# Performance work log

Hardware: AMD Instinct MI355X
Metric: run time of the kernel (lower is better)

## Reference

```python
import jax, jax.numpy as jnp
import numpy as np

B, N, M = 4, 16384, 4096
C1, C2 = 256, 512
C_IN = C1 + C2  # 768
C_H, C_OUT = 256, 256
EPS_BN = 1e-5
EPS_DIST = 1e-8


def _bn(x, gamma, beta):
    # x: [B, C, n]; training-mode batchnorm (batch statistics over B and n)
    mean = x.mean(axis=(0, 2), keepdims=True)
    var = x.var(axis=(0, 2), keepdims=True)
    return (x - mean) * jax.lax.rsqrt(var + EPS_BN) * gamma[None, :, None] + beta[None, :, None]


def setup_inputs() -> dict:
    key = jax.random.key(0)
    ks = jax.random.split(key, 8)
    inp = {
        "unknown": jax.random.normal(ks[0], (B, N, 3), dtype=jnp.float32),
        "known": jax.random.normal(ks[1], (B, M, 3), dtype=jnp.float32),
        "unknow_feats": jax.random.normal(ks[2], (B, C1, N), dtype=jnp.float32),
        "known_feats": jax.random.normal(ks[3], (B, C2, M), dtype=jnp.float32),
        "W1": jax.random.normal(ks[4], (C_H, C_IN), dtype=jnp.float32) * 0.02,
        "b1": jnp.zeros((C_H,), dtype=jnp.float32),
        "g1": jnp.ones((C_H,), dtype=jnp.float32),
        "bt1": jnp.zeros((C_H,), dtype=jnp.float32),
        "W2": jax.random.normal(ks[5], (C_OUT, C_H), dtype=jnp.float32) * 0.02,
        "b2": jnp.zeros((C_OUT,), dtype=jnp.float32),
        "g2": jnp.ones((C_OUT,), dtype=jnp.float32),
        "bt2": jnp.zeros((C_OUT,), dtype=jnp.float32),
    }
    return inp


def reference(unknown, known, unknow_feats, known_feats,
              W1, b1, g1, bt1, W2, b2, g2, bt2):
    # --- three_nn: brute-force squared distances [B, n, m], take 3 smallest ---
    d2 = jnp.sum((unknown[:, :, None, :] - known[:, None, :, :]) ** 2, axis=-1)
    neg_d, idx = jax.lax.top_k(-d2, 3)          # idx: [B, n, 3]
    dist = -neg_d                                # squared dists (as in CUDA three_nn)
    recip = 1.0 / (dist + EPS_DIST)
    weight = recip / recip.sum(axis=-1, keepdims=True)  # [B, n, 3]
    # --- three_interpolate: weighted gather from known_feats [B, C2, m] ---
    gathered = jax.vmap(lambda f, i: f[:, i])(known_feats, idx)  # [B, C2, n, 3]
    interp = jnp.einsum('bcnk,bnk->bcn', gathered, weight)       # [B, C2, n]
    # --- concat + SharedMLP (1x1 conv -> BN -> ReLU, twice) ---
    x = jnp.concatenate([interp, unknow_feats], axis=1)          # [B, C1+C2, n]
    x = jax.nn.relu(_bn(jnp.einsum('bcn,oc->bon', x, W1) + b1[None, :, None], g1, bt1))
    x = jax.nn.relu(_bn(jnp.einsum('bcn,oc->bon', x, W2) + b2[None, :, None], g2, bt2))
    return x  # [B, mlp[-1], n]
```

## Files before the change

kernel.cpp:

```cpp
#include <hip/hip_runtime.h>
#include <hip/hip_bf16.h>
#include <stdint.h>
#include <stddef.h>

#define B_   4
#define N_   16384
#define M_   4096
#define C1_  256
#define C2_  512
#define CIN_ 768
#define CH_  256
#define NG_  (B_*N_)
#define NSLOT 64

typedef __attribute__((ext_vector_type(8))) short short8;
typedef __attribute__((ext_vector_type(4))) float f32x4;

__device__ __forceinline__ float bf2f(unsigned short u){
  union { unsigned int i; float f; } v; v.i = ((unsigned int)u)<<16; return v.f;
}
__device__ __forceinline__ unsigned short f2bf(float f){
  union { float f; unsigned int i; } v; v.f = f;
  unsigned int r = v.i + 0x7fffu + ((v.i>>16)&1u);
  return (unsigned short)(r>>16);
}

__global__ __launch_bounds__(256) void prep_k(const float* __restrict__ W1,
                                              const float* __restrict__ W2,
                                              const float* __restrict__ kn,
                                              unsigned short* __restrict__ W1b,
                                              unsigned short* __restrict__ W2b,
                                              float4* __restrict__ k4){
  int i = blockIdx.x*256 + threadIdx.x;
  if (i < CIN_*CH_) W1b[i] = f2bf(W1[i]);
  if (i < CH_*CH_)  W2b[i] = f2bf(W2[i]);
  if (i < B_*M_){
    float x = kn[3*i], y = kn[3*i+1], z = kn[3*i+2];
    float4 v; v.x = -2.f*x; v.y = -2.f*y; v.z = -2.f*z; v.w = x*x+y*y+z*z;
    k4[i] = v;
  }
}

__global__ __launch_bounds__(256) void kft_k(const float* __restrict__ kf,
                                             unsigned short* __restrict__ kftb){
  int m0 = blockIdx.x*64, c0 = blockIdx.y*64, b = blockIdx.z;
  __shared__ float tile[64][65];
  int t = threadIdx.x;
  #pragma unroll
  for (int p=0;p<16;p++){
    int row = p*4 + (t>>6), col = t&63;
    tile[row][col] = kf[((size_t)b*C2_ + c0+row)*M_ + m0+col];
  }
  __syncthreads();
  #pragma unroll
  for (int q=0;q<2;q++){
    int id = q*256 + t;
    int ml = id >> 3, c8 = (id & 7)*8;
    short8 o;
    #pragma unroll
    for (int e=0;e<8;++e) o[e] = (short)f2bf(tile[c8+e][ml]);
    *(short8*)(kftb + ((size_t)b*M_ + m0+ml)*C2_ + c0 + c8) = o;
  }
}

__global__ __launch_bounds__(512) void three_nn_k(const float* __restrict__ unk,
                                                  const float4* __restrict__ k4,
                                                  int* __restrict__ idx,
                                                  float* __restrict__ wgt){
  __shared__ __align__(16) char smem[65536];
  float4* kl = (float4*)smem;
  float*  sd = (float*)smem;
  int*    si = (int*)(smem + 24*128*4);
  int b  = blockIdx.x >> 7;
  int n0 = (blockIdx.x & 127) * 128;
  int t = threadIdx.x;
  int w = t >> 6, l = t & 63;
  const float4* src = k4 + (size_t)b*M_;
  #pragma unroll
  for (int i=0;i<8;++i) kl[i*512 + t] = src[i*512 + t];
  const float* upA = unk + ((size_t)b*N_ + n0 + l)*3;
  const float* upB = unk + ((size_t)b*N_ + n0 + 64 + l)*3;
  float ax=upA[0], ay=upA[1], az=upA[2];
  float bx=upB[0], by=upB[1], bz=upB[2];
  __syncthreads();
  float a0=1e30f,a1=1e30f,a2=1e30f; int ia0=0,ia1=0,ia2=0;
  float b0=1e30f,b1=1e30f,b2=1e30f; int ib0=0,ib1=0,ib2=0;
  const float4* kp = kl + w*512;
  const int mbase = w*512;
  #pragma unroll 8
  for (int m=0;m<512;++m){
    float4 kq = kp[m];
    int mi = mbase + m;
    float da = __builtin_fmaf(ax,kq.x, __builtin_fmaf(ay,kq.y, __builtin_fmaf(az,kq.z, kq.w)));
    float db = __builtin_fmaf(bx,kq.x, __builtin_fmaf(by,kq.y, __builtin_fmaf(bz,kq.z, kq.w)));
    {
      bool c0 = da < a0, c1 = da < a1, c2 = da < a2;
      int tA = c1 ? ia1 : mi;  ia2 = c2 ? tA : ia2;
      int tB = c0 ? ia0 : mi;  ia1 = c1 ? tB : ia1;
      ia0 = c0 ? mi : ia0;
      float n1 = __builtin_amdgcn_fmed3f(da, a0, a1);
      float n2 = __builtin_amdgcn_fmed3f(da, a1, a2);
      a0 = fminf(da, a0); a1 = n1; a2 = n2;
    }
    {
      bool c0 = db < b0, c1 = db < b1, c2 = db < b2;
      int tA = c1 ? ib1 : mi;  ib2 = c2 ? tA : ib2;
      int tB = c0 ? ib0 : mi;  ib1 = c1 ? tB : ib1;
      ib0 = c0 ? mi : ib0;
      float n1 = __builtin_amdgcn_fmed3f(db, b0, b1);
      float n2 = __builtin_amdgcn_fmed3f(db, b1, b2);
      b0 = fminf(db, b0); b1 = n1; b2 = n2;
    }
  }
  __syncthreads();
  sd[(w*3+0)*128 + l] = a0;  sd[(w*3+0)*128 + 64 + l] = b0;
  sd[(w*3+1)*128 + l] = a1;  sd[(w*3+1)*128 + 64 + l] = b1;
  sd[(w*3+2)*128 + l] = a2;  sd[(w*3+2)*128 + 64 + l] = b2;
  si[(w*3+0)*128 + l] = ia0; si[(w*3+0)*128 + 64 + l] = ib0;
  si[(w*3+1)*128 + l] = ia1; si[(w*3+1)*128 + 64 + l] = ib1;
  si[(w*3+2)*128 + l] = ia2; si[(w*3+2)*128 + 64 + l] = ib2;
  __syncthreads();
  if (t < 128) {
    float bd0=1e30f,bd1=1e30f,bd2=1e30f; int bi0=0,bi1=0,bi2=0;
    #pragma unroll
    for (int q=0;q<24;++q){
      float d = sd[q*128 + t]; int ii = si[q*128 + t];
      bool c0 = d < bd0, c1 = d < bd1, c2 = d < bd2;
      int tA = c1 ? bi1 : ii;  bi2 = c2 ? tA : bi2;
      int tB = c0 ? bi0 : ii;  bi1 = c1 ? tB : bi1;
      bi0 = c0 ? ii : bi0;
      float nd1 = __builtin_amdgcn_fmed3f(d, bd0, bd1);
      float nd2 = __builtin_amdgcn_fmed3f(d, bd1, bd2);
      bd0 = fminf(d, bd0); bd1 = nd1; bd2 = nd2;
    }
    int np = n0 + t;
    const float* upt = unk + ((size_t)b*N_ + np)*3;
    float x = upt[0], y = upt[1], z = upt[2];
    float uu0 = x*x + y*y + z*z;
    float t0 = fmaxf(bd0 + uu0, 0.f) + 1e-8f;
    float t1 = fmaxf(bd1 + uu0, 0.f) + 1e-8f;
    float t2 = fmaxf(bd2 + uu0, 0.f) + 1e-8f;
    float r0 = 1.f/t0, r1 = 1.f/t1, r2 = 1.f/t2;
    float s = r0+r1+r2;
    size_t gp = ((size_t)b*N_ + np)*3;
    idx[gp]=bi0; idx[gp+1]=bi1; idx[gp+2]=bi2;
    wgt[gp]=r0/s; wgt[gp+1]=r1/s; wgt[gp+2]=r2/s;
  }
}

__global__ __launch_bounds__(256) void build_xt_k(const float* __restrict__ uf,
                                                  const unsigned short* __restrict__ kftb,
                                                  const int* __restrict__ idx,
                                                  const float* __restrict__ wgt,
                                                  unsigned short* __restrict__ Xt){
  int b  = blockIdx.x >> 8;
  int n0 = (blockIdx.x & 255) * 64;
  int t = threadIdx.x;
  __shared__ float tile[64][65];
  for (int cc=0; cc<4; ++cc){
    int c0 = cc*64;
    __syncthreads();
    #pragma unroll
    for (int p=0;p<16;p++){
      int row = p*4 + (t>>6), col = t&63;
      tile[row][col] = uf[((size_t)b*C1_ + c0+row)*N_ + n0+col];
    }
    __syncthreads();
    #pragma unroll
    for (int q=0;q<2;q++){
      int id = q*256 + t;
      int nl = id >> 3, c8 = (id & 7)*8;
      short8 o;
      #pragma unroll
      for (int e=0;e<8;++e) o[e] = (short)f2bf(tile[c8+e][nl]);
      *(short8*)(Xt + ((size_t)b*N_ + n0+nl)*CIN_ + C2_ + c0 + c8) = o;
    }
  }
  int w = t>>6, l = t&63;
  for (int i=0;i<16;++i){
    int n = n0 + w*16 + i;
    size_t gp = ((size_t)b*N_ + n)*3;
    int   j0 = idx[gp],   j1 = idx[gp+1],   j2 = idx[gp+2];
    float w0 = wgt[gp],   w1 = wgt[gp+1],   w2 = wgt[gp+2];
    const short8 a0 = *(const short8*)(kftb + ((size_t)b*M_ + j0)*C2_ + l*8);
    const short8 a1 = *(const short8*)(kftb + ((size_t)b*M_ + j1)*C2_ + l*8);
    const short8 a2 = *(const short8*)(kftb + ((size_t)b*M_ + j2)*C2_ + l*8);
    short8 o;
    #pragma unroll
    for (int e=0;e<8;++e){
      float f = w0*bf2f((unsigned short)a0[e])
              + w1*bf2f((unsigned short)a1[e])
              + w2*bf2f((unsigned short)a2[e]);
      o[e] = (short)f2bf(f);
    }
    *(short8*)(Xt + ((size_t)b*N_ + n)*CIN_ + l*8) = o;
  }
}

template<int KTOT, bool AFF>
__global__ __launch_bounds__(256) void gemm_bt_k(const unsigned short* __restrict__ Wb,
                                                 const unsigned short* __restrict__ Bt,
                                                 unsigned short* __restrict__ Yt,
                                                 float* __restrict__ sump,
                                                 float* __restrict__ sqp,
                                                 const float* __restrict__ scalep,
                                                 const float* __restrict__ shiftp){
  __shared__ short lsA[128*64];
  __shared__ short lsB[128*64];
  const int t = threadIdx.x, w = t>>6, l = t&63;
  const int nBase = blockIdx.x*128, oBase = blockIdx.y*128;
  const int wm = w>>1, wn = w&1, rl = l&15, hi = l>>4;
  f32x4 acc[4][4];
  #pragma unroll
  for (int i=0;i<4;i++)
    #pragma unroll
    for (int j=0;j<4;j++) acc[i][j] = (f32x4){0.f,0.f,0.f,0.f};
  const int srow8 = l>>3, sch = l&7;
  for (int ks=0; ks<KTOT/64; ++ks){
    const int k0 = ks*64;
    __syncthreads();
    #pragma unroll
    for (int j=0;j<4;++j){
      int row = w*8 + j*32 + srow8;
      const unsigned short* gA = Wb + (size_t)(oBase+row)*KTOT + k0 + ((sch ^ (row&7))<<3);
      __builtin_amdgcn_global_load_lds((const __attribute__((address_space(1))) unsigned int*)gA,
          (__attribute__((address_space(3))) unsigned int*)(lsA + w*512 + j*2048), 16, 0, 0);
      if constexpr (!AFF){
        const unsigned short* gB = Bt + (size_t)(nBase+row)*KTOT + k0 + ((sch ^ (row&7))<<3);
        __builtin_amdgcn_global_load_lds((const __attribute__((address_space(1))) unsigned int*)gB,
            (__attribute__((address_space(3))) unsigned int*)(lsB + w*512 + j*2048), 16, 0, 0);
      }
    }
    if constexpr (AFF){
      #pragma unroll
      for (int j=0;j<4;++j){
        int row = w*8 + j*32 + srow8;
        int chb = k0 + ((sch ^ (row&7))<<3);
        const short8 v = *(const short8*)(Bt + (size_t)(nBase+row)*KTOT + chb);
        float4 sc0 = *(const float4*)(scalep + chb);
        float4 sc1 = *(const float4*)(scalep + chb + 4);
        float4 sh0 = *(const float4*)(shiftp + chb);
        float4 sh1 = *(const float4*)(shiftp + chb + 4);
        short8 o;
        float f0 = bf2f((unsigned short)v[0])*sc0.x + sh0.x; o[0] = (short)f2bf(f0 > 0.f ? f0 : 0.f);
        float f1 = bf2f((unsigned short)v[1])*sc0.y + sh0.y; o[1] = (short)f2bf(f1 > 0.f ? f1 : 0.f);
        float f2 = bf2f((unsigned short)v[2])*sc0.z + sh0.z; o[2] = (short)f2bf(f2 > 0.f ? f2 : 0.f);
        float f3 = bf2f((unsigned short)v[3])*sc0.w + sh0.w; o[3] = (short)f2bf(f3 > 0.f ? f3 : 0.f);
        float f4 = bf2f((unsigned short)v[4])*sc1.x + sh1.x; o[4] = (short)f2bf(f4 > 0.f ? f4 : 0.f);
        float f5 = bf2f((unsigned short)v[5])*sc1.y + sh1.y; o[5] = (short)f2bf(f5 > 0.f ? f5 : 0.f);
        float f6 = bf2f((unsigned short)v[6])*sc1.z + sh1.z; o[6] = (short)f2bf(f6 > 0.f ? f6 : 0.f);
        float f7 = bf2f((unsigned short)v[7])*sc1.w + sh1.w; o[7] = (short)f2bf(f7 > 0.f ? f7 : 0.f);
        *(short8*)(lsB + w*512 + j*2048 + l*8) = o;
      }
    }
    __syncthreads();
    #pragma unroll
    for (int kk=0;kk<2;++kk){
      short8 af[4], bfr[4];
      const int pc = ((kk*4 + hi) ^ (rl&7)) << 3;
      #pragma unroll
      for (int mi=0;mi<4;++mi) af[mi]  = *(const short8*)(lsA + (wm*64 + mi*16 + rl)*64 + pc);
      #pragma unroll
      for (int ni=0;ni<4;++ni) bfr[ni] = *(const short8*)(lsB + (wn*64 + ni*16 + rl)*64 + pc);
      #pragma unroll
      for (int mi=0;mi<4;++mi)
        #pragma unroll
        for (int ni=0;ni<4;++ni)
          acc[mi][ni] = __builtin_amdgcn_mfma_f32_16x16x32_bf16(af[mi], bfr[ni], acc[mi][ni], 0,0,0);
    }
  }
  #pragma unroll
  for (int mi=0;mi<4;++mi)
    #pragma unroll
    for (int ni=0;ni<4;++ni){
      int n = nBase + wn*64 + ni*16 + rl;
      int o = oBase + wm*64 + mi*16 + hi*4;
      unsigned int lo = (unsigned int)f2bf(acc[mi][ni][0]) | ((unsigned int)f2bf(acc[mi][ni][1])<<16);
      unsigned int hi2= (unsigned int)f2bf(acc[mi][ni][2]) | ((unsigned int)f2bf(acc[mi][ni][3])<<16);
      uint2 vv; vv.x = lo; vv.y = hi2;
      *(uint2*)(Yt + (size_t)n*256 + o) = vv;
    }
  float s_[4][4], q_[4][4];
  #pragma unroll
  for (int mi=0;mi<4;++mi)
    #pragma unroll
    for (int j=0;j<4;++j){
      float s0 = acc[mi][0][j] + acc[mi][1][j] + acc[mi][2][j] + acc[mi][3][j];
      float q0 = acc[mi][0][j]*acc[mi][0][j];
      q0 = __builtin_fmaf(acc[mi][1][j], acc[mi][1][j], q0);
      q0 = __builtin_fmaf(acc[mi][2][j], acc[mi][2][j], q0);
      q0 = __builtin_fmaf(acc[mi][3][j], acc[mi][3][j], q0);
      s_[mi][j] = s0; q_[mi][j] = q0;
    }
  #pragma unroll
  for (int off=1; off<16; off<<=1){
    #pragma unroll
    for (int mi=0;mi<4;++mi)
      #pragma unroll
      for (int j=0;j<4;++j){
        s_[mi][j] += __shfl_xor(s_[mi][j], off);
        q_[mi][j] += __shfl_xor(q_[mi][j], off);
      }
  }
  if (rl == 0){
    const int slot = blockIdx.x & (NSLOT-1);
    #pragma unroll
    for (int mi=0;mi<4;++mi)
      #pragma unroll
      for (int j=0;j<4;++j){
        int o = oBase + wm*64 + mi*16 + hi*4 + j;
        atomicAdd(&sump[slot*256 + o], s_[mi][j]);
        atomicAdd(&sqp[slot*256 + o],  q_[mi][j]);
      }
  }
}

__global__ __launch_bounds__(256) void finalize_k(const float* __restrict__ sump,
                                                  const float* __restrict__ sqp,
                                                  const float* __restrict__ g,
                                                  const float* __restrict__ bt,
                                                  float* __restrict__ scale,
                                                  float* __restrict__ shift){
  int t = threadIdx.x;
  float s = 0.f, q = 0.f;
  #pragma unroll 8
  for (int k=0;k<NSLOT;++k){
    s += sump[k*256 + t];
    q += sqp[k*256 + t];
  }
  float mean = s * (1.f/65536.f);
  float var  = q * (1.f/65536.f) - mean*mean;
  float sc = g[t] * rsqrtf(var + 1e-5f);
  scale[t] = sc;
  shift[t] = bt[t] - mean*sc;
}

__global__ __launch_bounds__(256) void out_k(const unsigned short* __restrict__ Yt,
                                             const float* __restrict__ scale,
                                             const float* __restrict__ shift,
                                             float* __restrict__ out){
  int gn0 = blockIdx.x*64;
  int o0  = blockIdx.y*64;
  int b = gn0 >> 14, n0 = gn0 & (N_-1);
  __shared__ unsigned short tile[64][66];
  int t = threadIdx.x;
  #pragma unroll
  for (int p=0;p<4;++p){
    int nl = p*16 + (t>>4), ol = (t&15)*4;
    const unsigned short* src = Yt + (size_t)(gn0+nl)*256 + o0 + ol;
    uint2 vv = *(const uint2*)src;
    tile[nl][ol+0] = (unsigned short)(vv.x & 0xffff);
    tile[nl][ol+1] = (unsigned short)(vv.x >> 16);
    tile[nl][ol+2] = (unsigned short)(vv.y & 0xffff);
    tile[nl][ol+3] = (unsigned short)(vv.y >> 16);
  }
  __syncthreads();
  #pragma unroll
  for (int p=0;p<4;++p){
    int ol = p*16 + (t>>4), nl = (t&15)*4;
    float sc = scale[o0+ol], sh = shift[o0+ol];
    float4 r;
    float f0 = bf2f(tile[nl+0][ol])*sc + sh; r.x = f0 > 0.f ? f0 : 0.f;
    float f1 = bf2f(tile[nl+1][ol])*sc + sh; r.y = f1 > 0.f ? f1 : 0.f;
    float f2v= bf2f(tile[nl+2][ol])*sc + sh; r.z = f2v > 0.f ? f2v : 0.f;
    float f3 = bf2f(tile[nl+3][ol])*sc + sh; r.w = f3 > 0.f ? f3 : 0.f;
    *(float4*)(out + ((size_t)(b*256 + o0+ol))*N_ + n0 + nl) = r;
  }
}

extern "C" void kernel_launch(void* const* d_in, const int* in_sizes, int n_in,
                              void* d_out, int out_size, void* d_ws, size_t ws_size,
                              hipStream_t stream) {
  const float* unknown     = (const float*)d_in[0];
  const float* known       = (const float*)d_in[1];
  const float* unknow_f    = (const float*)d_in[2];
  const float* known_f     = (const float*)d_in[3];
  const float* W1          = (const float*)d_in[4];
  const float* g1          = (const float*)d_in[6];
  const float* bt1         = (const float*)d_in[7];
  const float* W2          = (const float*)d_in[8];
  const float* g2          = (const float*)d_in[10];
  const float* bt2         = (const float*)d_in[11];
  float* out = (float*)d_out;

  char* ws = (char*)d_ws;
  const size_t szXt   = (size_t)B_*N_*CIN_*2;
  const size_t szY    = (size_t)NG_*256*2;
  const size_t szKftb = (size_t)B_*M_*C2_*2;
  const size_t szIdx  = (size_t)NG_*3*4;
  const size_t szPart = (size_t)NSLOT*256*4;
  const size_t o_Xt   = 0;
  const size_t o_Y    = szXt;
  const size_t o_kftb = o_Y + szY;
  const size_t o_idx  = o_kftb + szKftb;
  const size_t o_wgt  = o_idx + szIdx;
  const size_t o_W1b  = o_wgt + szIdx;
  const size_t o_W2b  = o_W1b + (size_t)CIN_*CH_*2;
  const size_t o_st   = o_W2b + (size_t)CH_*CH_*2;
  const size_t o_k4   = o_st + 4*szPart + 4*256*sizeof(float);

  unsigned short* Xt   = (unsigned short*)(ws + o_Xt);
  unsigned short* Y2   = (unsigned short*)(ws + o_Xt);
  unsigned short* Y    = (unsigned short*)(ws + o_Y);
  unsigned short* kftb = (unsigned short*)(ws + o_kftb);
  int*            idx  = (int*)(ws + o_idx);
  float*          wgt  = (float*)(ws + o_wgt);
  unsigned short* W1b  = (unsigned short*)(ws + o_W1b);
  unsigned short* W2b  = (unsigned short*)(ws + o_W2b);
  float* st = (float*)(ws + o_st);
  float4* k4 = (float4*)(ws + o_k4);
  float *sum1p = st;
  float *sq1p  = st + NSLOT*256;
  float *sum2p = st + 2*NSLOT*256;
  float *sq2p  = st + 3*NSLOT*256;
  float *scale1 = st + 4*NSLOT*256;
  float *shift1 = scale1 + 256;
  float *scale2 = scale1 + 512;
  float *shift2 = scale1 + 768;

  hipMemsetAsync(st, 0, 4*szPart, stream);

  prep_k<<<768, 256, 0, stream>>>(W1, W2, known, W1b, W2b, k4);
  kft_k<<<dim3(M_/64, C2_/64, B_), 256, 0, stream>>>(known_f, kftb);
  three_nn_k<<<B_*(N_/128), 512, 0, stream>>>(unknown, k4, idx, wgt);
  build_xt_k<<<B_*(N_/64), 256, 0, stream>>>(unknow_f, kftb, idx, wgt, Xt);

  gemm_bt_k<CIN_, false><<<dim3(NG_/128, 2), 256, 0, stream>>>(W1b, Xt, Y, sum1p, sq1p, nullptr, nullptr);
  finalize_k<<<1, 256, 0, stream>>>(sum1p, sq1p, g1, bt1, scale1, shift1);

  gemm_bt_k<CH_, true><<<dim3(NG_/128, 2), 256, 0, stream>>>(W2b, Y, Y2, sum2p, sq2p, scale1, shift1);
  finalize_k<<<1, 256, 0, stream>>>(sum2p, sq2p, g2, bt2, scale2, shift2);
  out_k<<<dim3(NG_/64, 4), 256, 0, stream>>>(Y2, scale2, shift2, out);
}
```

Measured before the change: 287.0 us.

## Fuse three_interpolate gather into first GEMM's B-tile loading

The interpolated features are no longer materialized into a large concatenated Xt buffer. The first GEMM now gathers the three neighbor rows of known_feats, blends them by weight and writes the result straight into LDS for the first 512 K-columns. The unknown features are still transposed into a smaller buffer and loaded asynchronously. The grid is flattened so paired output-channel blocks run adjacently and share the same N tile in cache. This removes the write and re-read of the interpolated half of Xt, but the interpolation is now recomputed for each of the two output-channel blocks and uses synchronous loads inside the GEMM loop.

```diff
diff --git a/kernel.cpp b/kernel.cpp
--- a/kernel.cpp
+++ b/kernel.cpp
@@ -148,11 +148,8 @@
   }
 }
 
-__global__ __launch_bounds__(256) void build_xt_k(const float* __restrict__ uf,
-                                                  const unsigned short* __restrict__ kftb,
-                                                  const int* __restrict__ idx,
-                                                  const float* __restrict__ wgt,
-                                                  unsigned short* __restrict__ Xt){
+__global__ __launch_bounds__(256) void uft_k(const float* __restrict__ uf,
+                                             unsigned short* __restrict__ uft){
   int b  = blockIdx.x >> 8;
   int n0 = (blockIdx.x & 255) * 64;
   int t = threadIdx.x;
@@ -173,42 +170,26 @@
       short8 o;
       #pragma unroll
       for (int e=0;e<8;++e) o[e] = (short)f2bf(tile[c8+e][nl]);
-      *(short8*)(Xt + ((size_t)b*N_ + n0+nl)*CIN_ + C2_ + c0 + c8) = o;
-    }
-  }
-  int w = t>>6, l = t&63;
-  for (int i=0;i<16;++i){
-    int n = n0 + w*16 + i;
-    size_t gp = ((size_t)b*N_ + n)*3;
-    int   j0 = idx[gp],   j1 = idx[gp+1],   j2 = idx[gp+2];
-    float w0 = wgt[gp],   w1 = wgt[gp+1],   w2 = wgt[gp+2];
-    const short8 a0 = *(const short8*)(kftb + ((size_t)b*M_ + j0)*C2_ + l*8);
-    const short8 a1 = *(const short8*)(kftb + ((size_t)b*M_ + j1)*C2_ + l*8);
-    const short8 a2 = *(const short8*)(kftb + ((size_t)b*M_ + j2)*C2_ + l*8);
-    short8 o;
-    #pragma unroll
-    for (int e=0;e<8;++e){
-      float f = w0*bf2f((unsigned short)a0[e])
-              + w1*bf2f((unsigned short)a1[e])
-              + w2*bf2f((unsigned short)a2[e]);
-      o[e] = (short)f2bf(f);
-    }
-    *(short8*)(Xt + ((size_t)b*N_ + n)*CIN_ + l*8) = o;
-  }
-}
-
-template<int KTOT, bool AFF>
+      *(short8*)(uft + ((size_t)b*N_ + n0+nl)*CH_ + c0 + c8) = o;
+    }
+  }
+}
+
+template<int KTOT, int MODE>
 __global__ __launch_bounds__(256) void gemm_bt_k(const unsigned short* __restrict__ Wb,
                                                  const unsigned short* __restrict__ Bt,
                                                  unsigned short* __restrict__ Yt,
                                                  float* __restrict__ sump,
                                                  float* __restrict__ sqp,
                                                  const float* __restrict__ scalep,
-                                                 const float* __restrict__ shiftp){
+                                                 const float* __restrict__ shiftp,
+                                                 const unsigned short* __restrict__ kftb,
+                                                 const int* __restrict__ idx,
+                                                 const float* __restrict__ wgt){
   __shared__ short lsA[128*64];
   __shared__ short lsB[128*64];
   const int t = threadIdx.x, w = t>>6, l = t&63;
-  const int nBase = blockIdx.x*128, oBase = blockIdx.y*128;
+  const int nBase = (blockIdx.x>>1)*128, oBase = (blockIdx.x&1)*128;
   const int wm = w>>1, wn = w&1, rl = l&15, hi = l>>4;
   f32x4 acc[4][4];
   #pragma unroll
@@ -216,6 +197,19 @@
     #pragma unroll
     for (int j=0;j<4;j++) acc[i][j] = (f32x4){0.f,0.f,0.f,0.f};
   const int srow8 = l>>3, sch = l&7;
+  int jj0[4], jj1[4], jj2[4];
+  float ww0[4], ww1[4], ww2[4];
+  const unsigned short* kfb = nullptr;
+  if constexpr (MODE == 1){
+    kfb = kftb + (size_t)(nBase >> 14)*M_*C2_;
+    #pragma unroll
+    for (int j=0;j<4;++j){
+      int row = w*8 + j*32 + srow8;
+      size_t gp = (size_t)(nBase + row)*3;
+      jj0[j] = idx[gp];   jj1[j] = idx[gp+1];   jj2[j] = idx[gp+2];
+      ww0[j] = wgt[gp];   ww1[j] = wgt[gp+1];   ww2[j] = wgt[gp+2];
+    }
+  }
   for (int ks=0; ks<KTOT/64; ++ks){
     const int k0 = ks*64;
     __syncthreads();
@@ -225,13 +219,37 @@
       const unsigned short* gA = Wb + (size_t)(oBase+row)*KTOT + k0 + ((sch ^ (row&7))<<3);
       __builtin_amdgcn_global_load_lds((const __attribute__((address_space(1))) unsigned int*)gA,
           (__attribute__((address_space(3))) unsigned int*)(lsA + w*512 + j*2048), 16, 0, 0);
-      if constexpr (!AFF){
-        const unsigned short* gB = Bt + (size_t)(nBase+row)*KTOT + k0 + ((sch ^ (row&7))<<3);
-        __builtin_amdgcn_global_load_lds((const __attribute__((address_space(1))) unsigned int*)gB,
-            (__attribute__((address_space(3))) unsigned int*)(lsB + w*512 + j*2048), 16, 0, 0);
+      if constexpr (MODE == 1){
+        if (k0 >= C2_){
+          const unsigned short* gB = Bt + (size_t)(nBase+row)*CH_ + (k0 - C2_) + ((sch ^ (row&7))<<3);
+          __builtin_amdgcn_global_load_lds((const __attribute__((address_space(1))) unsigned int*)gB,
+              (__attribute__((address_space(3))) unsigned int*)(lsB + w*512 + j*2048), 16, 0, 0);
+        }
       }
     }
-    if constexpr (AFF){
+    if constexpr (MODE == 1){
+      if (k0 < C2_){
+        #pragma unroll
+        for (int j=0;j<4;++j){
+          int row = w*8 + j*32 + srow8;
+          int chb = k0 + ((sch ^ (row&7))<<3);
+          const short8 a0 = *(const short8*)(kfb + (size_t)jj0[j]*C2_ + chb);
+          const short8 a1 = *(const short8*)(kfb + (size_t)jj1[j]*C2_ + chb);
+          const short8 a2 = *(const short8*)(kfb + (size_t)jj2[j]*C2_ + chb);
+          float w0 = ww0[j], w1 = ww1[j], w2 = ww2[j];
+          short8 o;
+          #pragma unroll
+          for (int e=0;e<8;++e){
+            float f = w0*bf2f((unsigned short)a0[e])
+                    + w1*bf2f((unsigned short)a1[e])
+                    + w2*bf2f((unsigned short)a2[e]);
+            o[e] = (short)f2bf(f);
+          }
+          *(short8*)(lsB + w*512 + j*2048 + l*8) = o;
+        }
+      }
+    }
+    if constexpr (MODE == 2){
       #pragma unroll
       for (int j=0;j<4;++j){
         int row = w*8 + j*32 + srow8;
@@ -303,7 +321,7 @@
       }
   }
   if (rl == 0){
-    const int slot = blockIdx.x & (NSLOT-1);
+    const int slot = (blockIdx.x>>1) & (NSLOT-1);
     #pragma unroll
     for (int mi=0;mi<4;++mi)
       #pragma unroll
@@ -384,13 +402,13 @@
   float* out = (float*)d_out;
 
   char* ws = (char*)d_ws;
-  const size_t szXt   = (size_t)B_*N_*CIN_*2;
+  const size_t szUft  = (size_t)NG_*CH_*2;
   const size_t szY    = (size_t)NG_*256*2;
   const size_t szKftb = (size_t)B_*M_*C2_*2;
   const size_t szIdx  = (size_t)NG_*3*4;
   const size_t szPart = (size_t)NSLOT*256*4;
-  const size_t o_Xt   = 0;
-  const size_t o_Y    = szXt;
+  const size_t o_Uft  = 0;
+  const size_t o_Y    = szUft;
   const size_t o_kftb = o_Y + szY;
   const size_t o_idx  = o_kftb + szKftb;
   const size_t o_wgt  = o_idx + szIdx;
@@ -399,8 +417,8 @@
   const size_t o_st   = o_W2b + (size_t)CH_*CH_*2;
   const size_t o_k4   = o_st + 4*szPart + 4*256*sizeof(float);
 
-  unsigned short* Xt   = (unsigned short*)(ws + o_Xt);
-  unsigned short* Y2   = (unsigned short*)(ws + o_Xt);
+  unsigned short* Uft  = (unsigned short*)(ws + o_Uft);
+  unsigned short* Y2   = (unsigned short*)(ws + o_Uft);
   unsigned short* Y    = (unsigned short*)(ws + o_Y);
   unsigned short* kftb = (unsigned short*)(ws + o_kftb);
   int*            idx  = (int*)(ws + o_idx);
@@ -423,12 +441,14 @@
   prep_k<<<768, 256, 0, stream>>>(W1, W2, known, W1b, W2b, k4);
   kft_k<<<dim3(M_/64, C2_/64, B_), 256, 0, stream>>>(known_f, kftb);
   three_nn_k<<<B_*(N_/128), 512, 0, stream>>>(unknown, k4, idx, wgt);
-  build_xt_k<<<B_*(N_/64), 256, 0, stream>>>(unknow_f, kftb, idx, wgt, Xt);
-
-  gemm_bt_k<CIN_, false><<<dim3(NG_/128, 2), 256, 0, stream>>>(W1b, Xt, Y, sum1p, sq1p, nullptr, nullptr);
+  uft_k<<<B_*(N_/64), 256, 0, stream>>>(unknow_f, Uft);
+
+  gemm_bt_k<CIN_, 1><<<NG_/64, 256, 0, stream>>>(W1b, Uft, Y, sum1p, sq1p,
+                                                 nullptr, nullptr, kftb, idx, wgt);
   finalize_k<<<1, 256, 0, stream>>>(sum1p, sq1p, g1, bt1, scale1, shift1);
 
-  gemm_bt_k<CH_, true><<<dim3(NG_/128, 2), 256, 0, stream>>>(W2b, Y, Y2, sum2p, sq2p, scale1, shift1);
+  gemm_bt_k<CH_, 2><<<NG_/64, 256, 0, stream>>>(W2b, Y, Y2, sum2p, sq2p,
+                                                scale1, shift1, nullptr, nullptr, nullptr);
   finalize_k<<<1, 256, 0, stream>>>(sum2p, sq2p, g2, bt2, scale2, shift2);
   out_k<<<dim3(NG_/64, 4), 256, 0, stream>>>(Y2, scale2, shift2, out);
 }
```

New measurement: 259.3 us. 9.6% less time.
